# Optimization experiments

Measured on AMD Instinct MI355X. Metric: run time of the kernel, lower is better.

Reference implementation:

```python
import jax, jax.numpy as jnp
import numpy as np

B, T, I, H = 64, 1024, 256, 512
CLIP = 5.0


def setup_inputs() -> dict:
    key = jax.random.key(0)
    k0, k1, k2, k3 = jax.random.split(key, 4)
    x = jax.random.normal(k0, (B, T, I), dtype=jnp.float32)
    h0 = 0.1 * jax.random.normal(k1, (B, H), dtype=jnp.float32)
    # scale=True: ih_scale = I*(I+H)/I = I+H ; hh_scale = H*(I+H)/H = I+H
    std = 1.0 / np.sqrt(np.float32(I + H))
    W_ih = std * jax.random.normal(k2, (3 * H, I), dtype=jnp.float32)
    W_hh = std * jax.random.normal(k3, (3 * H, H), dtype=jnp.float32)
    # bias_ih: ones, last H entries zeroed; bias_hh: zeros (frozen)
    b_ih = jnp.concatenate([jnp.ones(2 * H, jnp.float32), jnp.zeros(H, jnp.float32)])
    b_hh = jnp.zeros(3 * H, jnp.float32)
    return {"x": x, "h0": h0, "W_ih": W_ih, "b_ih": b_ih, "W_hh": W_hh, "b_hh": b_hh}


def reference(x, h0, W_ih, b_ih, W_hh, b_hh):
    # Precompute input projections for all timesteps (same math, batched GEMM)
    x_all = jnp.einsum('bti,gi->btg', x, W_ih) + b_ih  # [B,T,3H]
    x_z, x_r, x_n = jnp.split(x_all, 3, axis=-1)       # each [B,T,H]
    W_zr, W_n = W_hh[: 2 * H], W_hh[2 * H:]
    b_zr, b_n = b_hh[: 2 * H], b_hh[2 * H:]

    def step(h, xs):
        xz, xr, xn = xs                                 # each [B,H]
        h_all = h @ W_zr.T + b_zr                       # [B,2H]
        hz, hr = jnp.split(h_all, 2, axis=-1)
        z = jax.nn.sigmoid(xz + hz)
        r = jax.nn.sigmoid(xr + hr)
        hn = (r * h) @ W_n.T + b_n
        n = jnp.tanh(xn + hn)
        h_new = jnp.clip(z * h + (1.0 - z) * n, -CLIP, CLIP)
        return h_new, h_new

    xs = (jnp.swapaxes(x_z, 0, 1), jnp.swapaxes(x_r, 0, 1), jnp.swapaxes(x_n, 0, 1))
    h_last, hs = jax.lax.scan(step, h0, xs)             # hs: [T,B,H]
    return jnp.swapaxes(hs, 0, 1), h_last
```

## Files before the change

kernel.cpp:

```cpp
#include <hip/hip_runtime.h>

#define BB   64
#define TT   1024
#define II   256
#define HH   512
#define NBLK 32
#define NTHR 512
#define SLICE 16
#define WHH_STR 520
#define WIH_STR 264
#define CLIPV 5.0f

typedef __attribute__((ext_vector_type(8))) short short8;
typedef __attribute__((ext_vector_type(4))) float f32x4;

__device__ __forceinline__ unsigned short f2bf(float f){
    unsigned u = __float_as_uint(f);
    u += 0x7fffu + ((u >> 16) & 1u);
    return (unsigned short)(u >> 16);
}
__device__ __forceinline__ float bf2f(unsigned short s){
    return __uint_as_float(((unsigned)s) << 16);
}
__device__ __forceinline__ unsigned packsplit(float f){
    unsigned short hi = f2bf(f);
    unsigned short lo = f2bf(f - bf2f(hi));
    return (unsigned)hi | ((unsigned)lo << 16);
}

__device__ __forceinline__ void unpack8(const uint4 a, const uint4 b, short8 &hi, short8 &lo){
    hi[0]=(short)a.x; lo[0]=(short)(a.x>>16);
    hi[1]=(short)a.y; lo[1]=(short)(a.y>>16);
    hi[2]=(short)a.z; lo[2]=(short)(a.z>>16);
    hi[3]=(short)a.w; lo[3]=(short)(a.w>>16);
    hi[4]=(short)b.x; lo[4]=(short)(b.x>>16);
    hi[5]=(short)b.y; lo[5]=(short)(b.y>>16);
    hi[6]=(short)b.z; lo[6]=(short)(b.z>>16);
    hi[7]=(short)b.w; lo[7]=(short)(b.w>>16);
}

#define SPLIT1(f, j) { float f_=(f); unsigned short h_=f2bf(f_); hi[j]=(short)h_; lo[j]=(short)f2bf(f_-bf2f(h_)); }
__device__ __forceinline__ void split8(const float4 a, const float4 b, short8 &hi, short8 &lo){
    SPLIT1(a.x,0) SPLIT1(a.y,1) SPLIT1(a.z,2) SPLIT1(a.w,3)
    SPLIT1(b.x,4) SPLIT1(b.y,5) SPLIT1(b.z,6) SPLIT1(b.w,7)
}
#undef SPLIT1

__device__ __forceinline__ f32x4 mfma(short8 a, short8 b, f32x4 c){
    return __builtin_amdgcn_mfma_f32_16x16x32_bf16(a, b, c, 0, 0, 0);
}

__device__ __forceinline__ uint4 aload4(const unsigned* p){
    const unsigned long long* q = (const unsigned long long*)p;
    unsigned long long a = __hip_atomic_load(q,   __ATOMIC_RELAXED, __HIP_MEMORY_SCOPE_AGENT);
    unsigned long long b = __hip_atomic_load(q+1, __ATOMIC_RELAXED, __HIP_MEMORY_SCOPE_AGENT);
    uint4 r; r.x=(unsigned)a; r.y=(unsigned)(a>>32); r.z=(unsigned)b; r.w=(unsigned)(b>>32);
    return r;
}
__device__ __forceinline__ void astore(unsigned* p, unsigned v){
    __hip_atomic_store(p, v, __ATOMIC_RELAXED, __HIP_MEMORY_SCOPE_AGENT);
}

__device__ __forceinline__ void wait_flags(const unsigned* f, unsigned target){
    int lane = threadIdx.x & 63;
    const unsigned* p = f + (lane & 31);
    while (true){
        unsigned v = __hip_atomic_load(p, __ATOMIC_RELAXED, __HIP_MEMORY_SCOPE_AGENT);
        if (__all((int)(v >= target))) break;
        __builtin_amdgcn_s_sleep(1);
    }
}

#define LDS_BYTES ((48*WHH_STR + 48*WIH_STR)*2*2 + 64*4 + 1024*4 + 1024*4)

extern "C" __global__ void pack_x_kernel(const float* __restrict__ x,
                                         unsigned* __restrict__ xp, int n){
    int idx = blockIdx.x * 256 + threadIdx.x;
    if (idx < n) xp[idx] = packsplit(x[idx]);
}

extern "C" __global__ void __launch_bounds__(NTHR, 2) gru_scan(
    const float* __restrict__ x,  const float* __restrict__ h0,
    const float* __restrict__ Wih, const float* __restrict__ bih,
    const float* __restrict__ Whh, const float* __restrict__ bhh,
    float* __restrict__ out, unsigned* __restrict__ ws,
    const unsigned* __restrict__ xp)
{
    extern __shared__ char smem[];
    unsigned short* whh_hi = (unsigned short*)smem;
    unsigned short* whh_lo = whh_hi + 48*WHH_STR;
    unsigned short* wih_hi = whh_lo + 48*WHH_STR;
    unsigned short* wih_lo = wih_hi + 48*WIH_STR;
    float* biasL = (float*)(wih_lo + 48*WIH_STR);
    float* nh1   = biasL + 64;
    float* h_lds = nh1 + 1024;

    unsigned* flagA = ws;
    unsigned* flagB = ws + 32;
    unsigned* hp    = ws + 128;
    unsigned* rhp   = hp + BB*HH;

    const int tid = threadIdx.x;
    const int bb  = blockIdx.x;
    const int colBase = SLICE * bb;

    for (int e = tid; e < 48*HH; e += NTHR){
        int r = e >> 9, k = e & (HH-1);
        int g = r >> 4, j = r & 15;
        int grow = g*HH + colBase + j;
        float v = Whh[grow*HH + k];
        unsigned short hv = f2bf(v);
        whh_hi[r*WHH_STR + k] = hv;
        whh_lo[r*WHH_STR + k] = f2bf(v - bf2f(hv));
    }
    for (int e = tid; e < 48*II; e += NTHR){
        int r = e >> 8, k = e & (II-1);
        int g = r >> 4, j = r & 15;
        int grow = g*HH + colBase + j;
        float v = Wih[grow*II + k];
        unsigned short hv = f2bf(v);
        wih_hi[r*WIH_STR + k] = hv;
        wih_lo[r*WIH_STR + k] = f2bf(v - bf2f(hv));
    }
    if (tid < 48){
        int g = tid >> 4, j = tid & 15;
        int grow = g*HH + colBase + j;
        biasL[tid] = bih[grow] + bhh[grow];
    }

    const int w = tid >> 6, lane = tid & 63;
    const int quad = lane >> 4, li = lane & 15;
    const int g = w >> 2, mt = w & 3;
    const int am  = mt*16 + li;
    const int cg  = colBase + li;
    const int dm0 = mt*16 + quad*4;

    for (int e = tid; e < BB*SLICE; e += NTHR){
        int m = e >> 4, c = e & 15;
        float v = h0[m*HH + colBase + c];
        astore(&hp[m*HH + colBase + c], packsplit(v));
        h_lds[m*16 + c] = v;
    }
    float hprev[4] = {0.f,0.f,0.f,0.f};
    if (g == 0){
        #pragma unroll
        for (int i = 0; i < 4; ++i) hprev[i] = h0[(size_t)(dm0+i)*HH + cg];
    }
    __syncthreads();
    if (tid == 0) __hip_atomic_fetch_add(flagB + bb, 1u, __ATOMIC_RELAXED, __HIP_MEMORY_SCOPE_AGENT);

    const float bsum = biasL[g*16 + li];
    const float bn   = biasL[32 + li];

    float zh[4], omz[4];
    f32x4 accNX;

    for (int t = 0; t < TT; ++t){
        uint4 xbuf[16];
        {
            const char* xb;
            if (xp) xb = (const char*)(xp + ((size_t)am*TT + t)*II + quad*8);
            else    xb = (const char*)(x  + ((size_t)am*TT + t)*II + quad*8);
            #pragma unroll
            for (int kt = 0; kt < 8; ++kt){
                xbuf[2*kt]   = *(const uint4*)(xb + (size_t)kt*128);
                xbuf[2*kt+1] = *(const uint4*)(xb + (size_t)kt*128 + 16);
            }
        }
        f32x4 accG = {0.f,0.f,0.f,0.f};
        accNX = (f32x4){0.f,0.f,0.f,0.f};
        #pragma unroll
        for (int kt = 0; kt < 8; ++kt){
            short8 ah, al;
            if (xp) unpack8(xbuf[2*kt], xbuf[2*kt+1], ah, al);
            else {
                float4 f0 = *(const float4*)&xbuf[2*kt];
                float4 f1 = *(const float4*)&xbuf[2*kt+1];
                split8(f0, f1, ah, al);
            }
            int ko = kt*32 + quad*8;
            short8 bh = *(const short8*)(wih_hi + (g*16+li)*WIH_STR + ko);
            short8 bl = *(const short8*)(wih_lo + (g*16+li)*WIH_STR + ko);
            accG = mfma(ah, bh, accG);
            accG = mfma(ah, bl, accG);
            accG = mfma(al, bh, accG);
            if (g == 0){
                short8 nbh = *(const short8*)(wih_hi + (32+li)*WIH_STR + ko);
                short8 nbl = *(const short8*)(wih_lo + (32+li)*WIH_STR + ko);
                accNX = mfma(ah, nbh, accNX);
                accNX = mfma(ah, nbl, accNX);
                accNX = mfma(al, nbh, accNX);
            }
        }

        if (w == 0) wait_flags(flagB, (unsigned)(t+1));
        __syncthreads();
        __builtin_amdgcn_sched_barrier(0);

        #pragma unroll
        for (int kt = 0; kt < 16; ++kt){
            int ko = kt*32 + quad*8;
            uint4 p0 = aload4(hp + am*HH + ko);
            uint4 p1 = aload4(hp + am*HH + ko + 4);
            short8 ah, al; unpack8(p0, p1, ah, al);
            short8 bh = *(const short8*)(whh_hi + (g*16+li)*WHH_STR + ko);
            short8 bl = *(const short8*)(whh_lo + (g*16+li)*WHH_STR + ko);
            accG = mfma(ah, bh, accG);
            accG = mfma(ah, bl, accG);
            accG = mfma(al, bh, accG);
        }
        {
            #pragma unroll
            for (int i = 0; i < 4; ++i){
                float hvf = (g == 0) ? hprev[i] : h_lds[(dm0+i)*16 + li];
                float gate = 1.f/(1.f + __expf(-(accG[i] + bsum)));
                if (g == 0){ zh[i] = gate*hvf; omz[i] = 1.f - gate; }
                else       { astore(&rhp[(dm0+i)*HH + cg], packsplit(gate*hvf)); }
            }
        }
        __syncthreads();
        if (tid == 0) __hip_atomic_fetch_add(flagA + bb, 1u, __ATOMIC_RELAXED, __HIP_MEMORY_SCOPE_AGENT);

        if (w == 0) wait_flags(flagA, (unsigned)(t+1));
        __syncthreads();
        __builtin_amdgcn_sched_barrier(0);

        f32x4 accN = (g == 0) ? accNX : (f32x4){0.f,0.f,0.f,0.f};
        #pragma unroll
        for (int kt8 = 0; kt8 < 8; ++kt8){
            int kt = g*8 + kt8;
            int ko = kt*32 + quad*8;
            uint4 p0 = aload4(rhp + am*HH + ko);
            uint4 p1 = aload4(rhp + am*HH + ko + 4);
            short8 ah, al; unpack8(p0, p1, ah, al);
            short8 bh = *(const short8*)(whh_hi + (32+li)*WHH_STR + ko);
            short8 bl = *(const short8*)(whh_lo + (32+li)*WHH_STR + ko);
            accN = mfma(ah, bh, accN);
            accN = mfma(ah, bl, accN);
            accN = mfma(al, bh, accN);
        }
        if (g == 1){
            #pragma unroll
            for (int i = 0; i < 4; ++i) nh1[(dm0+i)*16 + li] = accN[i];
        }
        __syncthreads();
        if (g == 0){
            #pragma unroll
            for (int i = 0; i < 4; ++i){
                float np = accN[i] + nh1[(dm0+i)*16 + li] + bn;
                float n  = tanhf(np);
                float hv = zh[i] + omz[i]*n;
                hv = fminf(fmaxf(hv, -CLIPV), CLIPV);
                hprev[i] = hv;
                astore(&hp[(dm0+i)*HH + cg], packsplit(hv));
                h_lds[(dm0+i)*16 + li] = hv;
            }
        }
        __syncthreads();
        if (tid == 0) __hip_atomic_fetch_add(flagB + bb, 1u, __ATOMIC_RELAXED, __HIP_MEMORY_SCOPE_AGENT);

        if (g == 0){
            #pragma unroll
            for (int i = 0; i < 4; ++i){
                out[((size_t)(dm0+i)*TT + t)*HH + cg] = hprev[i];
                if (t == TT-1) out[(size_t)BB*TT*HH + (size_t)(dm0+i)*HH + cg] = hprev[i];
            }
        }
    }
}

extern "C" void kernel_launch(void* const* d_in, const int* in_sizes, int n_in,
                              void* d_out, int out_size, void* d_ws, size_t ws_size,
                              hipStream_t stream) {
    const float* x   = (const float*)d_in[0];
    const float* h0  = (const float*)d_in[1];
    const float* Wih = (const float*)d_in[2];
    const float* bih = (const float*)d_in[3];
    const float* Whh = (const float*)d_in[4];
    const float* bhh = (const float*)d_in[5];
    float* out = (float*)d_out;
    unsigned* ws = (unsigned*)d_ws;

    const size_t base_bytes = 512 + 2*(size_t)BB*HH*4;
    const size_t xp_bytes   = (size_t)BB*TT*II*4;
    unsigned* xp = nullptr;
    if (ws_size >= base_bytes + xp_bytes){
        xp = ws + base_bytes/4;
        int n = BB*TT*II;
        pack_x_kernel<<<dim3((n + 255)/256), dim3(256), 0, stream>>>(x, xp, n);
    }
    hipMemsetAsync(d_ws, 0, 512, stream);
    (void)hipFuncSetAttribute((const void*)gru_scan,
                              hipFuncAttributeMaxDynamicSharedMemorySize,
                              (int)LDS_BYTES);
    gru_scan<<<dim3(NBLK), dim3(NTHR), LDS_BYTES, stream>>>(
        x, h0, Wih, bih, Whh, bhh, out, ws, xp);
}
```

Before: 28.40 ms.

## Partition GRU scan by batch across blocks, removing inter-block flag synchronization

```diff
diff --git a/kernel.cpp b/kernel.cpp
--- a/kernel.cpp
+++ b/kernel.cpp
@@ -4,12 +4,13 @@
 #define TT   1024
 #define II   256
 #define HH   512
-#define NBLK 32
+#define NBLK 4
 #define NTHR 512
-#define SLICE 16
-#define WHH_STR 520
-#define WIH_STR 264
 #define CLIPV 5.0f
+
+#define NKT  24
+#define WB_ELEMS (96*24*64*8)
+#define XA_DWORDS (BB*TT*II)
 
 typedef __attribute__((ext_vector_type(8))) short short8;
 typedef __attribute__((ext_vector_type(4))) float f32x4;
@@ -27,7 +28,6 @@
     unsigned short lo = f2bf(f - bf2f(hi));
     return (unsigned)hi | ((unsigned)lo << 16);
 }
-
 __device__ __forceinline__ void unpack8(const uint4 a, const uint4 b, short8 &hi, short8 &lo){
     hi[0]=(short)a.x; lo[0]=(short)(a.x>>16);
     hi[1]=(short)a.y; lo[1]=(short)(a.y>>16);
@@ -38,234 +38,209 @@
     hi[6]=(short)b.z; lo[6]=(short)(b.z>>16);
     hi[7]=(short)b.w; lo[7]=(short)(b.w>>16);
 }
-
 #define SPLIT1(f, j) { float f_=(f); unsigned short h_=f2bf(f_); hi[j]=(short)h_; lo[j]=(short)f2bf(f_-bf2f(h_)); }
 __device__ __forceinline__ void split8(const float4 a, const float4 b, short8 &hi, short8 &lo){
     SPLIT1(a.x,0) SPLIT1(a.y,1) SPLIT1(a.z,2) SPLIT1(a.w,3)
     SPLIT1(b.x,4) SPLIT1(b.y,5) SPLIT1(b.z,6) SPLIT1(b.w,7)
 }
 #undef SPLIT1
-
 __device__ __forceinline__ f32x4 mfma(short8 a, short8 b, f32x4 c){
     return __builtin_amdgcn_mfma_f32_16x16x32_bf16(a, b, c, 0, 0, 0);
 }
 
-__device__ __forceinline__ uint4 aload4(const unsigned* p){
-    const unsigned long long* q = (const unsigned long long*)p;
-    unsigned long long a = __hip_atomic_load(q,   __ATOMIC_RELAXED, __HIP_MEMORY_SCOPE_AGENT);
-    unsigned long long b = __hip_atomic_load(q+1, __ATOMIC_RELAXED, __HIP_MEMORY_SCOPE_AGENT);
-    uint4 r; r.x=(unsigned)a; r.y=(unsigned)(a>>32); r.z=(unsigned)b; r.w=(unsigned)(b>>32);
-    return r;
-}
-__device__ __forceinline__ void astore(unsigned* p, unsigned v){
-    __hip_atomic_store(p, v, __ATOMIC_RELAXED, __HIP_MEMORY_SCOPE_AGENT);
-}
-
-__device__ __forceinline__ void wait_flags(const unsigned* f, unsigned target){
-    int lane = threadIdx.x & 63;
-    const unsigned* p = f + (lane & 31);
-    while (true){
-        unsigned v = __hip_atomic_load(p, __ATOMIC_RELAXED, __HIP_MEMORY_SCOPE_AGENT);
-        if (__all((int)(v >= target))) break;
-        __builtin_amdgcn_s_sleep(1);
-    }
-}
-
-#define LDS_BYTES ((48*WHH_STR + 48*WIH_STR)*2*2 + 64*4 + 1024*4 + 1024*4)
-
-extern "C" __global__ void pack_x_kernel(const float* __restrict__ x,
-                                         unsigned* __restrict__ xp, int n){
-    int idx = blockIdx.x * 256 + threadIdx.x;
-    if (idx < n) xp[idx] = packsplit(x[idx]);
-}
+extern "C" __global__ void pack_w_kernel(const float* __restrict__ Wih,
+                                         const float* __restrict__ Whh,
+                                         unsigned short* __restrict__ wbh,
+                                         unsigned short* __restrict__ wbl){
+    int idx = blockIdx.x*256 + threadIdx.x;
+    if (idx >= WB_ELEMS) return;
+    int j = idx & 7, lane = (idx >> 3) & 63;
+    int tmp = idx >> 9;
+    int kt = tmp % 24, ct = tmp / 24;
+    int q = lane >> 4, li = lane & 15;
+    int gcol = ct*16 + li;
+    int k = kt*32 + q*8 + j;
+    float v = (k < HH) ? Whh[(size_t)gcol*HH + k] : Wih[(size_t)gcol*II + (k - HH)];
+    unsigned short hv = f2bf(v);
+    wbh[idx] = hv;
+    wbl[idx] = f2bf(v - bf2f(hv));
+}
+
+extern "C" __global__ void pack_xa_kernel(const float* __restrict__ x,
+                                          unsigned* __restrict__ xa){
+    int idx = blockIdx.x*256 + threadIdx.x;
+    if (idx >= XA_DWORDS) return;
+    int j = idx & 7, lane = (idx >> 3) & 63;
+    int kx = (idx >> 9) & 7, t = (idx >> 12) & 1023, bg = idx >> 22;
+    int q = lane >> 4, li = lane & 15;
+    int row = bg*16 + li, k = kx*32 + q*8 + j;
+    xa[idx] = packsplit(x[((size_t)row*TT + t)*II + k]);
+}
+
+#define LDS_BYTES 65536
 
 extern "C" __global__ void __launch_bounds__(NTHR, 2) gru_scan(
     const float* __restrict__ x,  const float* __restrict__ h0,
-    const float* __restrict__ Wih, const float* __restrict__ bih,
-    const float* __restrict__ Whh, const float* __restrict__ bhh,
-    float* __restrict__ out, unsigned* __restrict__ ws,
-    const unsigned* __restrict__ xp)
+    const float* __restrict__ bih, const float* __restrict__ bhh,
+    float* __restrict__ out,
+    const unsigned short* __restrict__ wbh,
+    const unsigned short* __restrict__ wbl,
+    const unsigned* __restrict__ xa)
 {
     extern __shared__ char smem[];
-    unsigned short* whh_hi = (unsigned short*)smem;
-    unsigned short* whh_lo = whh_hi + 48*WHH_STR;
-    unsigned short* wih_hi = whh_lo + 48*WHH_STR;
-    unsigned short* wih_lo = wih_hi + 48*WIH_STR;
-    float* biasL = (float*)(wih_lo + 48*WIH_STR);
-    float* nh1   = biasL + 64;
-    float* h_lds = nh1 + 1024;
-
-    unsigned* flagA = ws;
-    unsigned* flagB = ws + 32;
-    unsigned* hp    = ws + 128;
-    unsigned* rhp   = hp + BB*HH;
-
-    const int tid = threadIdx.x;
-    const int bb  = blockIdx.x;
-    const int colBase = SLICE * bb;
-
-    for (int e = tid; e < 48*HH; e += NTHR){
-        int r = e >> 9, k = e & (HH-1);
-        int g = r >> 4, j = r & 15;
-        int grow = g*HH + colBase + j;
-        float v = Whh[grow*HH + k];
-        unsigned short hv = f2bf(v);
-        whh_hi[r*WHH_STR + k] = hv;
-        whh_lo[r*WHH_STR + k] = f2bf(v - bf2f(hv));
+    uint4* hfr = (uint4*)smem;
+    uint4* rfr = hfr + 2048;
+
+    const int tid = threadIdx.x, bg = blockIdx.x;
+    const int w = tid >> 6, lane = tid & 63, quad = lane >> 4, li = lane & 15;
+
+    for (int it = 0; it < 16; ++it){
+        int d = it*NTHR + tid;
+        int dw = d & 3, u4i = d >> 2;
+        int lane2 = u4i & 63, plane = u4i >> 6;
+        int kt = plane >> 1, j4 = plane & 1;
+        int col = kt*32 + (lane2 >> 4)*8 + j4*4 + dw;
+        int row = lane2 & 15;
+        ((unsigned*)hfr)[d] = packsplit(h0[(size_t)(bg*16 + row)*HH + col]);
     }
-    for (int e = tid; e < 48*II; e += NTHR){
-        int r = e >> 8, k = e & (II-1);
-        int g = r >> 4, j = r & 15;
-        int grow = g*HH + colBase + j;
-        float v = Wih[grow*II + k];
-        unsigned short hv = f2bf(v);
-        wih_hi[r*WIH_STR + k] = hv;
-        wih_lo[r*WIH_STR + k] = f2bf(v - bf2f(hv));
-    }
-    if (tid < 48){
-        int g = tid >> 4, j = tid & 15;
-        int grow = g*HH + colBase + j;
-        biasL[tid] = bih[grow] + bhh[grow];
-    }
-
-    const int w = tid >> 6, lane = tid & 63;
-    const int quad = lane >> 4, li = lane & 15;
-    const int g = w >> 2, mt = w & 3;
-    const int am  = mt*16 + li;
-    const int cg  = colBase + li;
-    const int dm0 = mt*16 + quad*4;
-
-    for (int e = tid; e < BB*SLICE; e += NTHR){
-        int m = e >> 4, c = e & 15;
-        float v = h0[m*HH + colBase + c];
-        astore(&hp[m*HH + colBase + c], packsplit(v));
-        h_lds[m*16 + c] = v;
-    }
-    float hprev[4] = {0.f,0.f,0.f,0.f};
-    if (g == 0){
-        #pragma unroll
-        for (int i = 0; i < 4; ++i) hprev[i] = h0[(size_t)(dm0+i)*HH + cg];
+
+    float h_own[4][4], bz[4], br[4], bn_[4];
+    #pragma unroll
+    for (int c = 0; c < 4; ++c){
+        int col = w*64 + c*16 + li;
+        bz[c]  = bih[col]        + bhh[col];
+        br[c]  = bih[HH + col]   + bhh[HH + col];
+        bn_[c] = bih[2*HH + col] + bhh[2*HH + col];
+        #pragma unroll
+        for (int i = 0; i < 4; ++i)
+            h_own[c][i] = h0[(size_t)(bg*16 + quad*4 + i)*HH + col];
     }
     __syncthreads();
-    if (tid == 0) __hip_atomic_fetch_add(flagB + bb, 1u, __ATOMIC_RELAXED, __HIP_MEMORY_SCOPE_AGENT);
-
-    const float bsum = biasL[g*16 + li];
-    const float bn   = biasL[32 + li];
-
-    float zh[4], omz[4];
-    f32x4 accNX;
+
+    const int ctz0 = w*4, ctr0 = 32 + w*4, ctn0 = 64 + w*4;
+    float zh[4][4], omz[4][4];
 
     for (int t = 0; t < TT; ++t){
-        uint4 xbuf[16];
-        {
-            const char* xb;
-            if (xp) xb = (const char*)(xp + ((size_t)am*TT + t)*II + quad*8);
-            else    xb = (const char*)(x  + ((size_t)am*TT + t)*II + quad*8);
-            #pragma unroll
-            for (int kt = 0; kt < 8; ++kt){
-                xbuf[2*kt]   = *(const uint4*)(xb + (size_t)kt*128);
-                xbuf[2*kt+1] = *(const uint4*)(xb + (size_t)kt*128 + 16);
-            }
-        }
-        f32x4 accG = {0.f,0.f,0.f,0.f};
-        accNX = (f32x4){0.f,0.f,0.f,0.f};
-        #pragma unroll
-        for (int kt = 0; kt < 8; ++kt){
-            short8 ah, al;
-            if (xp) unpack8(xbuf[2*kt], xbuf[2*kt+1], ah, al);
-            else {
-                float4 f0 = *(const float4*)&xbuf[2*kt];
-                float4 f1 = *(const float4*)&xbuf[2*kt+1];
-                split8(f0, f1, ah, al);
-            }
-            int ko = kt*32 + quad*8;
-            short8 bh = *(const short8*)(wih_hi + (g*16+li)*WIH_STR + ko);
-            short8 bl = *(const short8*)(wih_lo + (g*16+li)*WIH_STR + ko);
-            accG = mfma(ah, bh, accG);
-            accG = mfma(ah, bl, accG);
-            accG = mfma(al, bh, accG);
-            if (g == 0){
-                short8 nbh = *(const short8*)(wih_hi + (32+li)*WIH_STR + ko);
-                short8 nbl = *(const short8*)(wih_lo + (32+li)*WIH_STR + ko);
-                accNX = mfma(ah, nbh, accNX);
-                accNX = mfma(ah, nbl, accNX);
-                accNX = mfma(al, nbh, accNX);
-            }
-        }
-
-        if (w == 0) wait_flags(flagB, (unsigned)(t+1));
+        f32x4 az[4], ar[4];
+        #pragma unroll
+        for (int c = 0; c < 4; ++c){ az[c] = (f32x4){0,0,0,0}; ar[c] = (f32x4){0,0,0,0}; }
+
+        #pragma unroll 2
+        for (int kt = 0; kt < 16; ++kt){
+            uint4 p0 = hfr[(kt*2+0)*64 + lane];
+            uint4 p1 = hfr[(kt*2+1)*64 + lane];
+            short8 ahi, alo; unpack8(p0, p1, ahi, alo);
+            #pragma unroll
+            for (int c = 0; c < 4; ++c){
+                int bi = (((ctz0+c)*NKT + kt)*64 + lane)*8;
+                short8 bh = *(const short8*)(wbh + bi);
+                short8 bl = *(const short8*)(wbl + bi);
+                az[c] = mfma(ahi,bh,az[c]); az[c] = mfma(ahi,bl,az[c]); az[c] = mfma(alo,bh,az[c]);
+            }
+            #pragma unroll
+            for (int c = 0; c < 4; ++c){
+                int bi = (((ctr0+c)*NKT + kt)*64 + lane)*8;
+                short8 bh = *(const short8*)(wbh + bi);
+                short8 bl = *(const short8*)(wbl + bi);
+                ar[c] = mfma(ahi,bh,ar[c]); ar[c] = mfma(ahi,bl,ar[c]); ar[c] = mfma(alo,bh,ar[c]);
+            }
+        }
+        #pragma unroll 2
+        for (int kx = 0; kx < 8; ++kx){
+            short8 ahi, alo;
+            if (xa){
+                const uint4* xp4 = (const uint4*)xa + ((((size_t)bg*TT + t)*8 + kx)*64 + lane)*2;
+                unpack8(xp4[0], xp4[1], ahi, alo);
+            } else {
+                const float* xb = x + ((size_t)(bg*16 + li)*TT + t)*II + kx*32 + quad*8;
+                split8(*(const float4*)xb, *(const float4*)(xb+4), ahi, alo);
+            }
+            int kt = 16 + kx;
+            #pragma unroll
+            for (int c = 0; c < 4; ++c){
+                int bi = (((ctz0+c)*NKT + kt)*64 + lane)*8;
+                short8 bh = *(const short8*)(wbh + bi);
+                short8 bl = *(const short8*)(wbl + bi);
+                az[c] = mfma(ahi,bh,az[c]); az[c] = mfma(ahi,bl,az[c]); az[c] = mfma(alo,bh,az[c]);
+            }
+            #pragma unroll
+            for (int c = 0; c < 4; ++c){
+                int bi = (((ctr0+c)*NKT + kt)*64 + lane)*8;
+                short8 bh = *(const short8*)(wbh + bi);
+                short8 bl = *(const short8*)(wbl + bi);
+                ar[c] = mfma(ahi,bh,ar[c]); ar[c] = mfma(ahi,bl,ar[c]); ar[c] = mfma(alo,bh,ar[c]);
+            }
+        }
+
+        #pragma unroll
+        for (int c = 0; c < 4; ++c){
+            int col = w*64 + c*16 + li;
+            int kt2 = col >> 5, j4 = (col >> 2) & 1, dwi = col & 3;
+            int lbase = ((kt2*2 + j4)*64 + ((col >> 3) & 3)*16 + quad*4);
+            #pragma unroll
+            for (int i = 0; i < 4; ++i){
+                float zv = 1.f/(1.f + __expf(-(az[c][i] + bz[c])));
+                zh[c][i] = zv*h_own[c][i]; omz[c][i] = 1.f - zv;
+                float rv = 1.f/(1.f + __expf(-(ar[c][i] + br[c])));
+                ((unsigned*)rfr)[(lbase + i)*4 + dwi] = packsplit(rv*h_own[c][i]);
+            }
+        }
         __syncthreads();
-        __builtin_amdgcn_sched_barrier(0);
-
-        #pragma unroll
+
+        f32x4 an[4];
+        #pragma unroll
+        for (int c = 0; c < 4; ++c) an[c] = (f32x4){0,0,0,0};
+
+        #pragma unroll 2
         for (int kt = 0; kt < 16; ++kt){
-            int ko = kt*32 + quad*8;
-            uint4 p0 = aload4(hp + am*HH + ko);
-            uint4 p1 = aload4(hp + am*HH + ko + 4);
-            short8 ah, al; unpack8(p0, p1, ah, al);
-            short8 bh = *(const short8*)(whh_hi + (g*16+li)*WHH_STR + ko);
-            short8 bl = *(const short8*)(whh_lo + (g*16+li)*WHH_STR + ko);
-            accG = mfma(ah, bh, accG);
-            accG = mfma(ah, bl, accG);
-            accG = mfma(al, bh, accG);
-        }
-        {
+            uint4 p0 = rfr[(kt*2+0)*64 + lane];
+            uint4 p1 = rfr[(kt*2+1)*64 + lane];
+            short8 ahi, alo; unpack8(p0, p1, ahi, alo);
+            #pragma unroll
+            for (int c = 0; c < 4; ++c){
+                int bi = (((ctn0+c)*NKT + kt)*64 + lane)*8;
+                short8 bh = *(const short8*)(wbh + bi);
+                short8 bl = *(const short8*)(wbl + bi);
+                an[c] = mfma(ahi,bh,an[c]); an[c] = mfma(ahi,bl,an[c]); an[c] = mfma(alo,bh,an[c]);
+            }
+        }
+        #pragma unroll 2
+        for (int kx = 0; kx < 8; ++kx){
+            short8 ahi, alo;
+            if (xa){
+                const uint4* xp4 = (const uint4*)xa + ((((size_t)bg*TT + t)*8 + kx)*64 + lane)*2;
+                unpack8(xp4[0], xp4[1], ahi, alo);
+            } else {
+                const float* xb = x + ((size_t)(bg*16 + li)*TT + t)*II + kx*32 + quad*8;
+                split8(*(const float4*)xb, *(const float4*)(xb+4), ahi, alo);
+            }
+            int kt = 16 + kx;
+            #pragma unroll
+            for (int c = 0; c < 4; ++c){
+                int bi = (((ctn0+c)*NKT + kt)*64 + lane)*8;
+                short8 bh = *(const short8*)(wbh + bi);
+                short8 bl = *(const short8*)(wbl + bi);
+                an[c] = mfma(ahi,bh,an[c]); an[c] = mfma(ahi,bl,an[c]); an[c] = mfma(alo,bh,an[c]);
+            }
+        }
+
+        #pragma unroll
+        for (int c = 0; c < 4; ++c){
+            int col = w*64 + c*16 + li;
+            int kt2 = col >> 5, j4 = (col >> 2) & 1, dwi = col & 3;
+            int lbase = ((kt2*2 + j4)*64 + ((col >> 3) & 3)*16 + quad*4);
             #pragma unroll
             for (int i = 0; i < 4; ++i){
-                float hvf = (g == 0) ? hprev[i] : h_lds[(dm0+i)*16 + li];
-                float gate = 1.f/(1.f + __expf(-(accG[i] + bsum)));
-                if (g == 0){ zh[i] = gate*hvf; omz[i] = 1.f - gate; }
-                else       { astore(&rhp[(dm0+i)*HH + cg], packsplit(gate*hvf)); }
+                float nv = tanhf(an[c][i] + bn_[c]);
+                float hv = zh[c][i] + omz[c][i]*nv;
+                hv = fminf(fmaxf(hv, -CLIPV), CLIPV);
+                h_own[c][i] = hv;
+                ((unsigned*)hfr)[(lbase + i)*4 + dwi] = packsplit(hv);
+                out[((size_t)(bg*16 + quad*4 + i)*TT + t)*HH + col] = hv;
+                if (t == TT-1) out[(size_t)BB*TT*HH + (size_t)(bg*16 + quad*4 + i)*HH + col] = hv;
             }
         }
         __syncthreads();
-        if (tid == 0) __hip_atomic_fetch_add(flagA + bb, 1u, __ATOMIC_RELAXED, __HIP_MEMORY_SCOPE_AGENT);
-
-        if (w == 0) wait_flags(flagA, (unsigned)(t+1));
-        __syncthreads();
-        __builtin_amdgcn_sched_barrier(0);
-
-        f32x4 accN = (g == 0) ? accNX : (f32x4){0.f,0.f,0.f,0.f};
-        #pragma unroll
-        for (int kt8 = 0; kt8 < 8; ++kt8){
-            int kt = g*8 + kt8;
-            int ko = kt*32 + quad*8;
-            uint4 p0 = aload4(rhp + am*HH + ko);
-            uint4 p1 = aload4(rhp + am*HH + ko + 4);
-            short8 ah, al; unpack8(p0, p1, ah, al);
-            short8 bh = *(const short8*)(whh_hi + (32+li)*WHH_STR + ko);
-            short8 bl = *(const short8*)(whh_lo + (32+li)*WHH_STR + ko);
-            accN = mfma(ah, bh, accN);
-            accN = mfma(ah, bl, accN);
-            accN = mfma(al, bh, accN);
-        }
-        if (g == 1){
-            #pragma unroll
-            for (int i = 0; i < 4; ++i) nh1[(dm0+i)*16 + li] = accN[i];
-        }
-        __syncthreads();
-        if (g == 0){
-            #pragma unroll
-            for (int i = 0; i < 4; ++i){
-                float np = accN[i] + nh1[(dm0+i)*16 + li] + bn;
-                float n  = tanhf(np);
-                float hv = zh[i] + omz[i]*n;
-                hv = fminf(fmaxf(hv, -CLIPV), CLIPV);
-                hprev[i] = hv;
-                astore(&hp[(dm0+i)*HH + cg], packsplit(hv));
-                h_lds[(dm0+i)*16 + li] = hv;
-            }
-        }
-        __syncthreads();
-        if (tid == 0) __hip_atomic_fetch_add(flagB + bb, 1u, __ATOMIC_RELAXED, __HIP_MEMORY_SCOPE_AGENT);
-
-        if (g == 0){
-            #pragma unroll
-            for (int i = 0; i < 4; ++i){
-                out[((size_t)(dm0+i)*TT + t)*HH + cg] = hprev[i];
-                if (t == TT-1) out[(size_t)BB*TT*HH + (size_t)(dm0+i)*HH + cg] = hprev[i];
-            }
-        }
     }
 }
 
@@ -279,20 +254,20 @@
     const float* Whh = (const float*)d_in[4];
     const float* bhh = (const float*)d_in[5];
     float* out = (float*)d_out;
-    unsigned* ws = (unsigned*)d_ws;
-
-    const size_t base_bytes = 512 + 2*(size_t)BB*HH*4;
-    const size_t xp_bytes   = (size_t)BB*TT*II*4;
-    unsigned* xp = nullptr;
-    if (ws_size >= base_bytes + xp_bytes){
-        xp = ws + base_bytes/4;
-        int n = BB*TT*II;
-        pack_x_kernel<<<dim3((n + 255)/256), dim3(256), 0, stream>>>(x, xp, n);
-    }
-    hipMemsetAsync(d_ws, 0, 512, stream);
+
+    const size_t WB_BYTES = (size_t)WB_ELEMS * 2;
+    unsigned short* wbh = (unsigned short*)d_ws;
+    unsigned short* wbl = wbh + WB_ELEMS;
+    unsigned* xa = nullptr;
+    if (ws_size >= 2*WB_BYTES + (size_t)XA_DWORDS*4)
+        xa = (unsigned*)((char*)d_ws + 2*WB_BYTES);
+
+    pack_w_kernel<<<dim3((WB_ELEMS + 255)/256), dim3(256), 0, stream>>>(Wih, Whh, wbh, wbl);
+    if (xa)
+        pack_xa_kernel<<<dim3((XA_DWORDS + 255)/256), dim3(256), 0, stream>>>(x, xa);
+
     (void)hipFuncSetAttribute((const void*)gru_scan,
-                              hipFuncAttributeMaxDynamicSharedMemorySize,
-                              (int)LDS_BYTES);
+                              hipFuncAttributeMaxDynamicSharedMemorySize, LDS_BYTES);
     gru_scan<<<dim3(NBLK), dim3(NTHR), LDS_BYTES, stream>>>(
-        x, h0, Wih, bih, Whh, bhh, out, ws, xp);
-}
+        x, h0, bih, bhh, out, wbh, wbl, xa);
+}
```

Result: slower. 104.5 ms (+268.0%).
